# Optimization experiments

Measured on AMD Instinct MI355X. Metric: run time of the kernel, lower is better.

## Reference

```python
import jax, jax.numpy as jnp
import numpy as np

# Dimensions (see shape_source)
N, M, C = 64, 300, 768          # batch, tokens (=max_frames), token dim
LAMB, G, K = 2, 8, 64           # expansion, groups, clusters
GS = LAMB * C // G              # group_size = 192
DESC = K * GS                   # 12288 NeXtVLAD descriptor dim
NB, NCLS = 512, 701             # bottleneck, classes


def setup_inputs() -> dict:
    key = jax.random.key(0)
    ks = jax.random.split(key, 8)
    w = lambda i, shape: jax.random.normal(ks[i], shape, jnp.float32) * 0.02
    return {
        "features": jax.random.normal(ks[0], (N, M + 1, C), jnp.float32),
        # NeXtVLAD_block params
        "fc0_w": w(1, (LAMB * C, C)), "fc0_b": jnp.zeros((LAMB * C,), jnp.float32),
        "fcgk_w": w(2, (G * K, LAMB * C)), "fcgk_b": jnp.zeros((G * K,), jnp.float32),
        "fcg_w": w(3, (G, LAMB * C)), "fcg_b": jnp.zeros((G,), jnp.float32),
        "bn0_g": jnp.ones((M,), jnp.float32), "bn0_b": jnp.zeros((M,), jnp.float32),
        "cw2": jax.random.uniform(ks[4], (1, GS, K), jnp.float32),
        "bn1_g": jnp.ones((1,), jnp.float32), "bn1_b": jnp.zeros((1,), jnp.float32),
        # ClassBlock params (Linear -> BN -> Linear classifier)
        "cls_fc_w": w(5, (NB, DESC)), "cls_fc_b": jnp.zeros((NB,), jnp.float32),
        "cls_bn_g": jnp.ones((NB,), jnp.float32), "cls_bn_b": jnp.zeros((NB,), jnp.float32),
        "cls_w": w(6, (NCLS, NB)), "cls_b": jnp.zeros((NCLS,), jnp.float32),
    }


def reference(features, fc0_w, fc0_b, fcgk_w, fcgk_b, fcg_w, fcg_b,
              bn0_g, bn0_b, cw2, bn1_g, bn1_b,
              cls_fc_w, cls_fc_b, cls_bn_g, cls_bn_b, cls_w, cls_b):
    # Drop CLS token -> local descriptors (N, M, C). (transpose+vector2image
    # in the torch code is a pure rearrangement back to (N, M, C) tokens.)
    x = features[:, 1:]
    # 1) expand D -> lamb*D
    x_dot = jnp.einsum('nmc,ec->nme', x, fc0_w) + fc0_b           # (N, M, lamb*C)
    # 2) group: (N, M*G, group_size)
    x_tilde = x_dot.reshape(-1, M * G, GS)
    # 3) soft assignment logits, BN over the frame axis (inference-mode BN:
    #    running stats 0/1 -> pure per-frame affine), softmax over clusters
    WgkX = jnp.einsum('nme,fe->nmf', x_dot, fcgk_w) + fcgk_b      # (N, M, G*K)
    WgkX = WgkX * bn0_g[None, :, None] + bn0_b[None, :, None]
    alpha_gk = jax.nn.softmax(WgkX.reshape(-1, M * G, K), axis=-1)
    # 4) sigmoid group attention
    alpha_g = jax.nn.sigmoid(jnp.einsum('nme,ge->nmg', x_dot, fcg_w) + fcg_b)
    alpha_g = alpha_g.reshape(-1, M * G, 1)
    activation = alpha_gk * alpha_g                                # (N, M*G, K)
    # 5) aggregate residuals: vlad = act^T x_tilde - a_sum * centers
    a = jnp.sum(activation, axis=1, keepdims=True) * cw2           # (N, GS, K)
    vlad = jnp.einsum('npk,npd->ndk', activation, x_tilde) - a     # (N, GS, K)
    # 6) L1-normalize over group_size dim (F.normalize(vlad, 1): p=1, dim=1)
    norm = jnp.maximum(jnp.sum(jnp.abs(vlad), axis=1, keepdims=True), 1e-12)
    vlad = (vlad / norm).reshape(-1, DESC)
    # bn1 = BatchNorm1d(1), inference mode -> scalar affine
    vlad = vlad * bn1_g[0] + bn1_b[0]
    # ClassBlock: Linear -> BN (inference affine) -> classifier Linear
    f = jnp.einsum('nd,bd->nb', vlad, cls_fc_w) + cls_fc_b         # (N, NB)
    f = f * cls_bn_g + cls_bn_b
    cls = jnp.einsum('nb,cb->nc', f, cls_w) + cls_b                # (N, NCLS)
    return (cls, f)
```

## Files before the change

### kernel.cpp

```cpp
#include <hip/hip_runtime.h>
#include <hip/hip_bf16.h>

#define NN 64
#define MM 300
#define CC 768
#define EE 1536
#define GG 8
#define KK 64
#define FF 512
#define GS 192
#define PP 2400
#define DESC 12288
#define NMROWS 19200
#define NB 512
#define NCLS 701

typedef _Float16 v8h __attribute__((ext_vector_type(8)));
typedef _Float16 v4h __attribute__((ext_vector_type(4)));
typedef float    v4f __attribute__((ext_vector_type(4)));

#define GLOAD_LDS16(g, s) \
    __builtin_amdgcn_global_load_lds( \
        (const __attribute__((address_space(1))) void*)(g), \
        (__attribute__((address_space(3))) void*)(s), 16, 0, 0)

__global__ __launch_bounds__(256)
void pack_x_k(const float* __restrict__ f, _Float16* __restrict__ o)
{
    int idx = blockIdx.x * 256 + threadIdx.x;
    int row = idx / 192;
    int c4  = (idx - row * 192) * 4;
    int n = row / 300, m = row - n * 300;
    float4 v = *(const float4*)(f + ((size_t)(n * 301 + m + 1)) * CC + c4);
    v4h h = { (_Float16)v.x, (_Float16)v.y, (_Float16)v.z, (_Float16)v.w };
    *(v4h*)(o + (size_t)row * CC + c4) = h;
}

__global__ __launch_bounds__(256)
void pack_w_k(const float* __restrict__ s, _Float16* __restrict__ o, int n4)
{
    int idx = blockIdx.x * 256 + threadIdx.x;
    if (idx >= n4) return;
    float4 v = *(const float4*)(s + (size_t)idx * 4);
    v4h h = { (_Float16)v.x, (_Float16)v.y, (_Float16)v.z, (_Float16)v.w };
    *(v4h*)(o + (size_t)idx * 4) = h;
}

__global__ __launch_bounds__(256)
void transpose_w1_k(const float* __restrict__ w1, _Float16* __restrict__ o)
{
    __shared__ float T[64][65];
    const int c0 = blockIdx.x * 64, e0 = blockIdx.y * 64;
    const int tc = threadIdx.x & 63, te = threadIdx.x >> 6;
    #pragma unroll
    for (int r = 0; r < 16; ++r) {
        int el = te * 16 + r;
        T[el][tc] = w1[(size_t)(e0 + el) * CC + c0 + tc];
    }
    __syncthreads();
    #pragma unroll
    for (int r = 0; r < 16; ++r) {
        int cl = te * 16 + r;
        o[(size_t)(c0 + cl) * EE + e0 + tc] = (_Float16)T[tc][cl];
    }
}

__global__ __launch_bounds__(256)
void biasc_k(const float* __restrict__ w2, const float* __restrict__ b2,
             const float* __restrict__ wg, const float* __restrict__ bg,
             const float* __restrict__ b0, float* __restrict__ biasc)
{
    int f = blockIdx.x;
    const float* row = (f < FF) ? (w2 + (size_t)f * EE) : (wg + (size_t)(f - FF) * EE);
    float s = 0.f;
    for (int e = threadIdx.x; e < EE; e += 256) s += row[e] * b0[e];
    __shared__ float red[256];
    red[threadIdx.x] = s;
    __syncthreads();
    for (int o = 128; o; o >>= 1) {
        if (threadIdx.x < o) red[threadIdx.x] += red[threadIdx.x + o];
        __syncthreads();
    }
    if (threadIdx.x == 0)
        biasc[f] = red[0] + ((f < FF) ? b2[f] : bg[f - FF]);
}

__global__ __launch_bounds__(256)
void wgc_k(const float* __restrict__ wg, const float* __restrict__ w1,
           float* __restrict__ wgc)
{
    const int c = blockIdx.x * 64 + (threadIdx.x & 63);
    const int q = threadIdx.x >> 6;
    float acc[GG] = {};
    for (int e = q * 384; e < q * 384 + 384; ++e) {
        float w1v = w1[(size_t)e * CC + c];
        #pragma unroll
        for (int g = 0; g < GG; ++g) acc[g] = fmaf(wg[g * EE + e], w1v, acc[g]);
    }
    __shared__ float red[4][GG][64];
    #pragma unroll
    for (int g = 0; g < GG; ++g) red[q][g][threadIdx.x & 63] = acc[g];
    __syncthreads();
    if (threadIdx.x < 64) {
        #pragma unroll
        for (int g = 0; g < GG; ++g)
            wgc[g * CC + c] = red[0][g][threadIdx.x] + red[1][g][threadIdx.x]
                            + red[2][g][threadIdx.x] + red[3][g][threadIdx.x];
    }
}

template<bool OUTF16, bool BN0, bool SOFTGATE, bool BIAS>
__global__ __launch_bounds__(256)
void hgemm_nt(const _Float16* __restrict__ A, const _Float16* __restrict__ B,
              const float* __restrict__ bias,
              const float* __restrict__ bn_g, const float* __restrict__ bn_b,
              const float* __restrict__ sig,
              void* __restrict__ Cout, int Ndim, int Kdim)
{
    __shared__ _Float16 As[128 * 32];
    __shared__ _Float16 Bs[128 * 32];

    const int tid  = threadIdx.x;
    const int wave = tid >> 6, lane = tid & 63;
    const int wr   = wave >> 1, wc = wave & 1;
    const int row0 = blockIdx.y * 128, col0 = blockIdx.x * 128;

    const int r0 = tid >> 2, cs = tid & 3;
    const int cc = cs ^ ((r0 >> 1) & 3);
    const _Float16* ga0 = A + (size_t)(row0 + r0) * Kdim + cc * 8;
    const _Float16* ga1 = A + (size_t)(row0 + r0 + 64) * Kdim + cc * 8;
    const _Float16* gb0 = B + (size_t)(col0 + r0) * Kdim + cc * 8;
    const _Float16* gb1 = B + (size_t)(col0 + r0 + 64) * Kdim + cc * 8;
    _Float16* sa0 = As + wave * 512;
    _Float16* sa1 = As + 2048 + wave * 512;
    _Float16* sb0 = Bs + wave * 512;
    _Float16* sb1 = Bs + 2048 + wave * 512;

    v4f acc[4][4];
    #pragma unroll
    for (int i = 0; i < 4; ++i)
        #pragma unroll
        for (int j = 0; j < 4; ++j)
            acc[i][j] = (v4f){0.f, 0.f, 0.f, 0.f};

    const int fm = lane & 15, fq = lane >> 4;
    const int sw = (fm >> 1) & 3;
    const _Float16* arp = As + (wr * 64 + fm) * 32 + (fq ^ sw) * 8;
    const _Float16* brp = Bs + (wc * 64 + fm) * 32 + (fq ^ sw) * 8;

    for (int kt = 0; kt < Kdim; kt += 32) {
        GLOAD_LDS16(ga0 + kt, sa0);
        GLOAD_LDS16(ga1 + kt, sa1);
        GLOAD_LDS16(gb0 + kt, sb0);
        GLOAD_LDS16(gb1 + kt, sb1);
        __syncthreads();

        v8h af[4], bf[4];
        #pragma unroll
        for (int i = 0; i < 4; ++i) af[i] = *(const v8h*)(arp + i * 16 * 32);
        #pragma unroll
        for (int j = 0; j < 4; ++j) bf[j] = *(const v8h*)(brp + j * 16 * 32);
        #pragma unroll
        for (int i = 0; i < 4; ++i)
            #pragma unroll
            for (int j = 0; j < 4; ++j)
                acc[i][j] = __builtin_amdgcn_mfma_f32_16x16x32_f16(
                    af[i], bf[j], acc[i][j], 0, 0, 0);
        __syncthreads();
    }

    float bj[4];
    #pragma unroll
    for (int j = 0; j < 4; ++j)
        bj[j] = BIAS ? bias[col0 + wc * 64 + j * 16 + fm] : 0.f;

    if (SOFTGATE) {
        const int gidx = (col0 >> 6) + wc;
        #pragma unroll
        for (int i = 0; i < 4; ++i) {
            #pragma unroll
            for (int r = 0; r < 4; ++r) {
                int grow = row0 + wr * 64 + i * 16 + fq * 4 + r;
                int n = grow / 300, mm = grow - n * 300;
                float g = bn_g[mm], bb = bn_b[mm];
                float v[4];
                #pragma unroll
                for (int j = 0; j < 4; ++j)
                    v[j] = (acc[i][j][r] + bj[j]) * g + bb;
                float mx = fmaxf(fmaxf(v[0], v[1]), fmaxf(v[2], v[3]));
                #pragma unroll
                for (int w = 1; w < 16; w <<= 1) mx = fmaxf(mx, __shfl_xor(mx, w));
                float e[4], s = 0.f;
                #pragma unroll
                for (int j = 0; j < 4; ++j) { e[j] = __expf(v[j] - mx); s += e[j]; }
                #pragma unroll
                for (int w = 1; w < 16; w <<= 1) s += __shfl_xor(s, w);
                float gate = sig[(size_t)grow * GG + gidx];
                float inv = gate / s;
                if (OUTF16) {
                    _Float16* cp = (_Float16*)Cout + (size_t)grow * Ndim + col0 + wc * 64;
                    #pragma unroll
                    for (int j = 0; j < 4; ++j) cp[j * 16 + fm] = (_Float16)(e[j] * inv);
                } else {
                    float* cp = (float*)Cout + (size_t)grow * Ndim + col0 + wc * 64;
                    #pragma unroll
                    for (int j = 0; j < 4; ++j) cp[j * 16 + fm] = e[j] * inv;
                }
            }
        }
        return;
    }

    #pragma unroll
    for (int i = 0; i < 4; ++i) {
        #pragma unroll
        for (int r = 0; r < 4; ++r) {
            int grow = row0 + wr * 64 + i * 16 + fq * 4 + r;
            float g = 1.f, bb = 0.f;
            if (BN0) { int m = grow % 300; g = bn_g[m]; bb = bn_b[m]; }
            #pragma unroll
            for (int j = 0; j < 4; ++j) {
                int gcol = col0 + wc * 64 + j * 16 + fm;
                float v = acc[i][j][r] + bj[j];
                if (BN0) v = v * g + bb;
                if (OUTF16)
                    ((_Float16*)Cout)[(size_t)grow * Ndim + gcol] = (_Float16)v;
                else
                    ((float*)Cout)[(size_t)grow * Ndim + gcol] = v;
            }
        }
    }
}

__global__ __launch_bounds__(256)
void alpha_sig_k(const _Float16* __restrict__ x, const float* __restrict__ wgc,
                 const float* __restrict__ bgc, float* __restrict__ sig)
{
    __shared__ float W[GG * CC];
    for (int i = threadIdx.x; i < GG * CC; i += 256) W[i] = wgc[i];
    __syncthreads();

    const int wave = threadIdx.x >> 6;
    const int lane = threadIdx.x & 63;

    for (int rr = 0; rr < 4; ++rr) {
        int row = blockIdx.x * 16 + wave * 4 + rr;
        const _Float16* xr = x + (size_t)row * CC;
        float acc[GG] = {};
        for (int c = lane; c < CC; c += 64) {
            float xv = (float)xr[c];
            #pragma unroll
            for (int g = 0; g < GG; ++g) acc[g] = fmaf(xv, W[g * CC + c], acc[g]);
        }
        float myval = 0.f;
        #pragma unroll
        for (int g = 0; g < GG; ++g) {
            float s = acc[g];
            #pragma unroll
            for (int o = 32; o; o >>= 1) s += __shfl_xor(s, o);
            if (lane == g) myval = s + bgc[g];
        }
        if (lane < GG) {
            sig[(size_t)row * GG + lane] = 1.f / (1.f + __expf(-myval));
        }
    }
}

__global__ __launch_bounds__(256)
void asum_ps_k(const _Float16* __restrict__ act, float* __restrict__ apart)
{
    const int ps = blockIdx.x, n = blockIdx.y;
    const int k = threadIdx.x & 63, q = threadIdx.x >> 6;
    const _Float16* base = act + ((size_t)n * PP + ps * 300 + q * 75) * 64 + k;
    float s = 0.f;
    for (int p = 0; p < 75; ++p) s += (float)base[(size_t)p * 64];
    __shared__ float part[4][64];
    part[q][k] = s;
    __syncthreads();
    if (threadIdx.x < 64)
        apart[((size_t)ps * NN + n) * 64 + threadIdx.x] =
            part[0][threadIdx.x] + part[1][threadIdx.x]
          + part[2][threadIdx.x] + part[3][threadIdx.x];
}

__global__ __launch_bounds__(256)
void vlad_ps_k(const _Float16* __restrict__ act, const _Float16* __restrict__ xdot,
               float* __restrict__ part)
{
    const int dt = blockIdx.x, n = blockIdx.y, ps = blockIdx.z;
    const int d0 = dt * 64;
    const int p0 = ps * 300, pend = p0 + 300;
    __shared__ float As[16][64];
    __shared__ float Xs[16][64];
    const int tid = threadIdx.x;
    const int tx = tid & 15, ty = tid >> 4;
    const int kb = tx * 4, db = ty * 4;
    const _Float16* actn = act + (size_t)n * PP * 64;
    const _Float16* xn   = xdot + (size_t)n * MM * EE;
    float acc[4][4] = {};

    const int lpp = tid >> 4, lk4 = (tid & 15) << 2;
    for (int pc = p0; pc < pend; pc += 16) {
        int p = pc + lpp;
        float a0 = 0.f, a1 = 0.f, a2 = 0.f, a3 = 0.f;
        float x0 = 0.f, x1 = 0.f, x2 = 0.f, x3 = 0.f;
        if (p < pend) {
            v4h avh = *(const v4h*)(actn + (size_t)p * 64 + lk4);
            a0 = (float)avh[0]; a1 = (float)avh[1]; a2 = (float)avh[2]; a3 = (float)avh[3];
            v4h xv = *(const v4h*)(xn + (size_t)(p >> 3) * EE + (p & 7) * GS + d0 + lk4);
            x0 = (float)xv[0]; x1 = (float)xv[1]; x2 = (float)xv[2]; x3 = (float)xv[3];
        }
        As[lpp][lk4 + 0] = a0; As[lpp][lk4 + 1] = a1;
        As[lpp][lk4 + 2] = a2; As[lpp][lk4 + 3] = a3;
        Xs[lpp][lk4 + 0] = x0; Xs[lpp][lk4 + 1] = x1;
        Xs[lpp][lk4 + 2] = x2; Xs[lpp][lk4 + 3] = x3;
        __syncthreads();
        #pragma unroll
        for (int q = 0; q < 16; ++q) {
            float4 a4 = *(const float4*)&As[q][kb];
            float4 x4 = *(const float4*)&Xs[q][db];
            float aa[4] = {a4.x, a4.y, a4.z, a4.w};
            float xx[4] = {x4.x, x4.y, x4.z, x4.w};
            #pragma unroll
            for (int i = 0; i < 4; ++i)
                #pragma unroll
                for (int j = 0; j < 4; ++j)
                    acc[i][j] = fmaf(xx[i], aa[j], acc[i][j]);
        }
        __syncthreads();
    }

    float* pp = part + ((size_t)ps * NN + n) * DESC;
    #pragma unroll
    for (int i = 0; i < 4; ++i) {
        int dd = d0 + db + i;
        float4 o = {acc[i][0], acc[i][1], acc[i][2], acc[i][3]};
        *(float4*)(pp + (size_t)dd * 64 + kb) = o;
    }
}

__global__ __launch_bounds__(256)
void vlad_reduce_k(const float* __restrict__ part, const float* __restrict__ apart,
                   const float* __restrict__ cw2, float* __restrict__ vlad)
{
    int idx = blockIdx.x * 256 + threadIdx.x;
    float s = 0.f;
    #pragma unroll
    for (int ps = 0; ps < 8; ++ps) s += part[(size_t)ps * (NN * DESC) + idx];
    int k = idx & 63;
    int d = (idx >> 6) % GS;
    int n = idx / DESC;
    float a = 0.f;
    #pragma unroll
    for (int ps = 0; ps < 8; ++ps) a += apart[((size_t)ps * NN + n) * 64 + k];
    vlad[idx] = s - a * cw2[d * 64 + k];
}

__global__ __launch_bounds__(256)
void norm_k(float* __restrict__ vlad, const float* __restrict__ bn1g,
            const float* __restrict__ bn1b)
{
    int n = blockIdx.x;
    float* v = vlad + (size_t)n * DESC;
    int k = threadIdx.x & 63, q = threadIdx.x >> 6;
    float s = 0.f;
    for (int d = q * 48; d < q * 48 + 48; ++d) s += fabsf(v[d * 64 + k]);
    __shared__ float part[4][64];
    __shared__ float inv[64];
    part[q][k] = s;
    __syncthreads();
    if (threadIdx.x < 64) {
        float t = part[0][threadIdx.x] + part[1][threadIdx.x]
                + part[2][threadIdx.x] + part[3][threadIdx.x];
        inv[threadIdx.x] = 1.f / fmaxf(t, 1e-12f);
    }
    __syncthreads();
    float g = bn1g[0], b = bn1b[0];
    for (int idx = threadIdx.x; idx < DESC; idx += 256) {
        v[idx] = v[idx] * inv[idx & 63] * g + b;
    }
}

__global__ __launch_bounds__(256)
void fsplit_k(const float* __restrict__ vlad, const float* __restrict__ W,
              float* __restrict__ part)
{
    const int bcol0 = (blockIdx.x & 7) * 64;
    const int ks = blockIdx.x >> 3;
    const int kc0 = ks * 256;
    __shared__ float Vs[32][68];
    __shared__ float Ws[32][68];
    const int tid = threadIdx.x, tx = tid & 15, ty = tid >> 4;
    float acc[4][4] = {};

    for (int kc = kc0; kc < kc0 + 256; kc += 32) {
        #pragma unroll
        for (int it = 0; it < 2; ++it) {
            int sl = tid + it * 256;
            int rr = sl >> 3, k4 = (sl & 7) << 2;
            float4 v = *(const float4*)(vlad + (size_t)rr * DESC + kc + k4);
            Vs[k4+0][rr] = v.x; Vs[k4+1][rr] = v.y; Vs[k4+2][rr] = v.z; Vs[k4+3][rr] = v.w;
            float4 w = *(const float4*)(W + (size_t)(bcol0 + rr) * DESC + kc + k4);
            Ws[k4+0][rr] = w.x; Ws[k4+1][rr] = w.y; Ws[k4+2][rr] = w.z; Ws[k4+3][rr] = w.w;
        }
        __syncthreads();
        #pragma unroll
        for (int q = 0; q < 32; ++q) {
            float4 wv = *(const float4*)&Ws[q][tx*4];
            float4 vv = *(const float4*)&Vs[q][ty*4];
            float wa[4] = {wv.x, wv.y, wv.z, wv.w};
            float va[4] = {vv.x, vv.y, vv.z, vv.w};
            #pragma unroll
            for (int i = 0; i < 4; ++i)
                #pragma unroll
                for (int j = 0; j < 4; ++j)
                    acc[i][j] = fmaf(va[i], wa[j], acc[i][j]);
        }
        __syncthreads();
    }
    float* p = part + (size_t)ks * (NN * NB);
    #pragma unroll
    for (int i = 0; i < 4; ++i) {
        int n = ty * 4 + i;
        float4 o = {acc[i][0], acc[i][1], acc[i][2], acc[i][3]};
        *(float4*)(p + (size_t)n * NB + bcol0 + tx*4) = o;
    }
}

__global__ __launch_bounds__(256)
void freduce_k(const float* __restrict__ part, const float* __restrict__ bias,
               const float* __restrict__ bng, const float* __restrict__ bnb,
               float* __restrict__ f)
{
    int idx = blockIdx.x * 256 + threadIdx.x;
    float s = 0.f;
    for (int ks = 0; ks < 48; ++ks) s += part[(size_t)ks * (NN * NB) + idx];
    int b = idx & (NB - 1);
    f[idx] = (s + bias[b]) * bng[b] + bnb[b];
}

__global__ __launch_bounds__(256)
void cls_k(const float* __restrict__ f, const float* __restrict__ W,
           const float* __restrict__ bias, float* __restrict__ out)
{
    const int c0 = blockIdx.x * 64;
    __shared__ float Fs[32][68];
    __shared__ float Ws[32][68];
    const int tid = threadIdx.x, tx = tid & 15, ty = tid >> 4;
    float acc[4][4] = {};

    for (int kc = 0; kc < NB; kc += 32) {
        #pragma unroll
        for (int it = 0; it < 2; ++it) {
            int sl = tid + it * 256;
            int rr = sl >> 3, k4 = (sl & 7) << 2;
            float4 v = *(const float4*)(f + (size_t)rr * NB + kc + k4);
            Fs[k4+0][rr] = v.x; Fs[k4+1][rr] = v.y; Fs[k4+2][rr] = v.z; Fs[k4+3][rr] = v.w;
            int c = c0 + rr;
            float4 w = (c < NCLS) ? *(const float4*)(W + (size_t)c * NB + kc + k4)
                                  : make_float4(0.f, 0.f, 0.f, 0.f);
            Ws[k4+0][rr] = w.x; Ws[k4+1][rr] = w.y; Ws[k4+2][rr] = w.z; Ws[k4+3][rr] = w.w;
        }
        __syncthreads();
        #pragma unroll
        for (int q = 0; q < 32; ++q) {
            float4 wv = *(const float4*)&Ws[q][tx*4];
            float4 fv = *(const float4*)&Fs[q][ty*4];
            float wa[4] = {wv.x, wv.y, wv.z, wv.w};
            float fa[4] = {fv.x, fv.y, fv.z, fv.w};
            #pragma unroll
            for (int i = 0; i < 4; ++i)
                #pragma unroll
                for (int j = 0; j < 4; ++j)
                    acc[i][j] = fmaf(fa[i], wa[j], acc[i][j]);
        }
        __syncthreads();
    }
    #pragma unroll
    for (int i = 0; i < 4; ++i) {
        int n = ty * 4 + i;
        #pragma unroll
        for (int j = 0; j < 4; ++j) {
            int c = c0 + tx * 4 + j;
            if (c < NCLS) out[(size_t)n * NCLS + c] = acc[i][j] + bias[c];
        }
    }
}

extern "C" void kernel_launch(void* const* d_in, const int* in_sizes, int n_in,
                              void* d_out, int out_size, void* d_ws, size_t ws_size,
                              hipStream_t stream)
{
    const float* features = (const float*)d_in[0];
    const float* fc0_w    = (const float*)d_in[1];
    const float* fc0_b    = (const float*)d_in[2];
    const float* fcgk_w   = (const float*)d_in[3];
    const float* fcgk_b   = (const float*)d_in[4];
    const float* fcg_w    = (const float*)d_in[5];
    const float* fcg_b    = (const float*)d_in[6];
    const float* bn0_g    = (const float*)d_in[7];
    const float* bn0_b    = (const float*)d_in[8];
    const float* cw2      = (const float*)d_in[9];
    const float* bn1_g    = (const float*)d_in[10];
    const float* bn1_b    = (const float*)d_in[11];
    const float* cls_fc_w = (const float*)d_in[12];
    const float* cls_fc_b = (const float*)d_in[13];
    const float* cls_bn_g = (const float*)d_in[14];
    const float* cls_bn_b = (const float*)d_in[15];
    const float* cls_w    = (const float*)d_in[16];
    const float* cls_b    = (const float*)d_in[17];

    char* ws = (char*)d_ws;
    _Float16* xf16   = (_Float16*)(ws + 0);
    _Float16* w1f16  = (_Float16*)(ws + 29491200);
    _Float16* w2f16  = (_Float16*)(ws + 31850496);
    _Float16* w1t16  = (_Float16*)(ws + 33423360);
    _Float16* w2cf16 = (_Float16*)(ws + 35782656);
    float*    biasc  = (float*)   (ws + 36569088);
    float*    wgc    = (float*)   (ws + 36573184);
    _Float16* xdot16 = (_Float16*)(ws + 36597760);
    _Float16* act16  = (_Float16*)(ws + 95580160);
    float*    sigma  = (float*)   (ws + 115240960);
    float*    apart  = (float*)   (ws + 115855360);
    float*    vpart  = (float*)   (ws + 115986432);
    float*    vlad   = (float*)   (ws + 141152256);
    float*    fpart  = (float*)   (ws + 144297984);

    float* cls_out = (float*)d_out;
    float* f_out   = cls_out + NN * NCLS;

    dim3 blk(256);

    pack_x_k<<<14400, blk, 0, stream>>>(features, xf16);
    pack_w_k<<<1152, blk, 0, stream>>>(fc0_w, w1f16, EE * CC / 4);
    pack_w_k<<<768, blk, 0, stream>>>(fcgk_w, w2f16, FF * EE / 4);
    transpose_w1_k<<<dim3(12, 24), blk, 0, stream>>>(fc0_w, w1t16);
    biasc_k<<<520, blk, 0, stream>>>(fcgk_w, fcgk_b, fcg_w, fcg_b, fc0_b, biasc);
    wgc_k<<<12, blk, 0, stream>>>(fcg_w, fc0_w, wgc);
    hgemm_nt<true, false, false, false><<<dim3(6, 4), blk, 0, stream>>>(
        w2f16, w1t16, nullptr, nullptr, nullptr, nullptr, w2cf16, CC, EE);

    hgemm_nt<true, false, false, true><<<dim3(12, 150), blk, 0, stream>>>(
        xf16, w1f16, fc0_b, nullptr, nullptr, nullptr, xdot16, EE, CC);

    alpha_sig_k<<<1200, blk, 0, stream>>>(xf16, wgc, biasc + FF, sigma);

    hgemm_nt<true, true, true, true><<<dim3(4, 150), blk, 0, stream>>>(
        xf16, w2cf16, biasc, bn0_g, bn0_b, sigma, act16, FF, CC);

    asum_ps_k<<<dim3(8, 64), blk, 0, stream>>>(act16, apart);

    vlad_ps_k<<<dim3(3, 64, 8), blk, 0, stream>>>(act16, xdot16, vpart);
    vlad_reduce_k<<<3072, blk, 0, stream>>>(vpart, apart, cw2, vlad);

    norm_k<<<64, blk, 0, stream>>>(vlad, bn1_g, bn1_b);

    fsplit_k<<<384, blk, 0, stream>>>(vlad, cls_fc_w, fpart);
    freduce_k<<<128, blk, 0, stream>>>(fpart, cls_fc_b, cls_bn_g, cls_bn_b, f_out);

    cls_k<<<11, blk, 0, stream>>>(f_out, cls_w, cls_b, cls_out);
}
```

Measured before the change: 510.7 us.

## Merge setup, alpha, asum and norm kernels; split-K cls and wgc with atomics

Folds the six setup kernels into one block-indexed setup kernel and gives wgc more parallelism through atomic accumulation. The alpha-sigmoid work rides as extra blocks in the xdot GEMM launch, and the activation-sum runs as extra blocks in the VLAD partial kernel. The VLAD reduce and L1 norm become one kernel, and the classifier is split over K with atomics. The aim is fewer launches and better occupancy of small kernels, at the cost of two memsets, float atomics and extra branch-indexed blocks.

Result: faster. 445.9 us (-12.7%).

```diff
diff --git a/kernel.cpp b/kernel.cpp
--- a/kernel.cpp
+++ b/kernel.cpp
@@ -25,105 +25,151 @@
         (__attribute__((address_space(3))) void*)(s), 16, 0, 0)
 
 __global__ __launch_bounds__(256)
-void pack_x_k(const float* __restrict__ f, _Float16* __restrict__ o)
-{
-    int idx = blockIdx.x * 256 + threadIdx.x;
-    int row = idx / 192;
-    int c4  = (idx - row * 192) * 4;
-    int n = row / 300, m = row - n * 300;
-    float4 v = *(const float4*)(f + ((size_t)(n * 301 + m + 1)) * CC + c4);
-    v4h h = { (_Float16)v.x, (_Float16)v.y, (_Float16)v.z, (_Float16)v.w };
-    *(v4h*)(o + (size_t)row * CC + c4) = h;
-}
-
-__global__ __launch_bounds__(256)
-void pack_w_k(const float* __restrict__ s, _Float16* __restrict__ o, int n4)
-{
-    int idx = blockIdx.x * 256 + threadIdx.x;
-    if (idx >= n4) return;
-    float4 v = *(const float4*)(s + (size_t)idx * 4);
-    v4h h = { (_Float16)v.x, (_Float16)v.y, (_Float16)v.z, (_Float16)v.w };
-    *(v4h*)(o + (size_t)idx * 4) = h;
-}
-
-__global__ __launch_bounds__(256)
-void transpose_w1_k(const float* __restrict__ w1, _Float16* __restrict__ o)
-{
-    __shared__ float T[64][65];
-    const int c0 = blockIdx.x * 64, e0 = blockIdx.y * 64;
-    const int tc = threadIdx.x & 63, te = threadIdx.x >> 6;
-    #pragma unroll
-    for (int r = 0; r < 16; ++r) {
-        int el = te * 16 + r;
-        T[el][tc] = w1[(size_t)(e0 + el) * CC + c0 + tc];
-    }
-    __syncthreads();
-    #pragma unroll
-    for (int r = 0; r < 16; ++r) {
-        int cl = te * 16 + r;
-        o[(size_t)(c0 + cl) * EE + e0 + tc] = (_Float16)T[tc][cl];
-    }
-}
-
-__global__ __launch_bounds__(256)
-void biasc_k(const float* __restrict__ w2, const float* __restrict__ b2,
-             const float* __restrict__ wg, const float* __restrict__ bg,
-             const float* __restrict__ b0, float* __restrict__ biasc)
-{
-    int f = blockIdx.x;
-    const float* row = (f < FF) ? (w2 + (size_t)f * EE) : (wg + (size_t)(f - FF) * EE);
-    float s = 0.f;
-    for (int e = threadIdx.x; e < EE; e += 256) s += row[e] * b0[e];
-    __shared__ float red[256];
-    red[threadIdx.x] = s;
-    __syncthreads();
-    for (int o = 128; o; o >>= 1) {
-        if (threadIdx.x < o) red[threadIdx.x] += red[threadIdx.x + o];
-        __syncthreads();
-    }
-    if (threadIdx.x == 0)
-        biasc[f] = red[0] + ((f < FF) ? b2[f] : bg[f - FF]);
-}
-
-__global__ __launch_bounds__(256)
-void wgc_k(const float* __restrict__ wg, const float* __restrict__ w1,
-           float* __restrict__ wgc)
-{
-    const int c = blockIdx.x * 64 + (threadIdx.x & 63);
-    const int q = threadIdx.x >> 6;
-    float acc[GG] = {};
-    for (int e = q * 384; e < q * 384 + 384; ++e) {
-        float w1v = w1[(size_t)e * CC + c];
-        #pragma unroll
-        for (int g = 0; g < GG; ++g) acc[g] = fmaf(wg[g * EE + e], w1v, acc[g]);
-    }
-    __shared__ float red[4][GG][64];
-    #pragma unroll
-    for (int g = 0; g < GG; ++g) red[q][g][threadIdx.x & 63] = acc[g];
-    __syncthreads();
-    if (threadIdx.x < 64) {
-        #pragma unroll
-        for (int g = 0; g < GG; ++g)
-            wgc[g * CC + c] = red[0][g][threadIdx.x] + red[1][g][threadIdx.x]
-                            + red[2][g][threadIdx.x] + red[3][g][threadIdx.x];
-    }
-}
-
-template<bool OUTF16, bool BN0, bool SOFTGATE, bool BIAS>
+void setup_k(const float* __restrict__ features, const float* __restrict__ fc0_w,
+             const float* __restrict__ fcgk_w, const float* __restrict__ fcg_w,
+             const float* __restrict__ fc0_b, const float* __restrict__ fcgk_b,
+             const float* __restrict__ fcg_b,
+             _Float16* __restrict__ xf16, _Float16* __restrict__ w1f16,
+             _Float16* __restrict__ w2f16, _Float16* __restrict__ w1t16,
+             float* __restrict__ biasc, float* __restrict__ wgc)
+{
+    __shared__ __align__(16) char sm[16640];
+    const int bid = blockIdx.x, tid = threadIdx.x;
+
+    if (bid < 14400) {
+        int idx = bid * 256 + tid;
+        int row = idx / 192;
+        int c4  = (idx - row * 192) * 4;
+        int n = row / 300, m = row - n * 300;
+        float4 v = *(const float4*)(features + ((size_t)(n * 301 + m + 1)) * CC + c4);
+        v4h h = { (_Float16)v.x, (_Float16)v.y, (_Float16)v.z, (_Float16)v.w };
+        *(v4h*)(xf16 + (size_t)row * CC + c4) = h;
+        return;
+    }
+    if (bid < 15552) {
+        int idx = (bid - 14400) * 256 + tid;
+        float4 v = *(const float4*)(fc0_w + (size_t)idx * 4);
+        v4h h = { (_Float16)v.x, (_Float16)v.y, (_Float16)v.z, (_Float16)v.w };
+        *(v4h*)(w1f16 + (size_t)idx * 4) = h;
+        return;
+    }
+    if (bid < 16320) {
+        int idx = (bid - 15552) * 256 + tid;
+        float4 v = *(const float4*)(fcgk_w + (size_t)idx * 4);
+        v4h h = { (_Float16)v.x, (_Float16)v.y, (_Float16)v.z, (_Float16)v.w };
+        *(v4h*)(w2f16 + (size_t)idx * 4) = h;
+        return;
+    }
+    if (bid < 16608) {
+        float (*T)[65] = (float(*)[65])sm;
+        int b = bid - 16320;
+        const int c0 = (b % 12) * 64, e0 = (b / 12) * 64;
+        const int tc = tid & 63, te = tid >> 6;
+        #pragma unroll
+        for (int r = 0; r < 16; ++r) {
+            int el = te * 16 + r;
+            T[el][tc] = fc0_w[(size_t)(e0 + el) * CC + c0 + tc];
+        }
+        __syncthreads();
+        #pragma unroll
+        for (int r = 0; r < 16; ++r) {
+            int cl = te * 16 + r;
+            w1t16[(size_t)(c0 + cl) * EE + e0 + tc] = (_Float16)T[tc][cl];
+        }
+        return;
+    }
+    if (bid < 17128) {
+        float* red = (float*)sm;
+        int f = bid - 16608;
+        const float* row = (f < FF) ? (fcgk_w + (size_t)f * EE)
+                                    : (fcg_w + (size_t)(f - FF) * EE);
+        float s = 0.f;
+        for (int e = tid; e < EE; e += 256) s += row[e] * fc0_b[e];
+        red[tid] = s;
+        __syncthreads();
+        for (int o = 128; o; o >>= 1) {
+            if (tid < o) red[tid] += red[tid + o];
+            __syncthreads();
+        }
+        if (tid == 0)
+            biasc[f] = red[0] + ((f < FF) ? fcgk_b[f] : fcg_b[f - FF]);
+        return;
+    }
+    {
+        float (*red)[GG][64] = (float(*)[GG][64])sm;
+        int b = bid - 17128;
+        const int c = (b % 12) * 64 + (tid & 63);
+        const int es = b / 12, q = tid >> 6;
+        float acc[GG] = {};
+        for (int e = es * 192 + q * 48; e < es * 192 + q * 48 + 48; ++e) {
+            float w1v = fc0_w[(size_t)e * CC + c];
+            #pragma unroll
+            for (int g = 0; g < GG; ++g) acc[g] = fmaf(fcg_w[g * EE + e], w1v, acc[g]);
+        }
+        #pragma unroll
+        for (int g = 0; g < GG; ++g) red[q][g][tid & 63] = acc[g];
+        __syncthreads();
+        if (tid < 64) {
+            #pragma unroll
+            for (int g = 0; g < GG; ++g) {
+                float v = red[0][g][tid] + red[1][g][tid] + red[2][g][tid] + red[3][g][tid];
+                atomicAdd(&wgc[g * CC + c], v);
+            }
+        }
+        return;
+    }
+}
+
+template<bool OUTF16, bool BN0, bool SOFTGATE, bool BIAS, bool ALPHA>
 __global__ __launch_bounds__(256)
 void hgemm_nt(const _Float16* __restrict__ A, const _Float16* __restrict__ B,
               const float* __restrict__ bias,
               const float* __restrict__ bn_g, const float* __restrict__ bn_b,
               const float* __restrict__ sig,
-              void* __restrict__ Cout, int Ndim, int Kdim)
-{
-    __shared__ _Float16 As[128 * 32];
-    __shared__ _Float16 Bs[128 * 32];
-
+              void* __restrict__ Cout, int Ndim, int Kdim, int gx,
+              int gemm_blocks,
+              const float* __restrict__ wgc, const float* __restrict__ bgc,
+              float* __restrict__ sigout)
+{
+    __shared__ __align__(16) char smem[24576];
     const int tid  = threadIdx.x;
+    const int bid  = blockIdx.x;
     const int wave = tid >> 6, lane = tid & 63;
-    const int wr   = wave >> 1, wc = wave & 1;
-    const int row0 = blockIdx.y * 128, col0 = blockIdx.x * 128;
+
+    if (ALPHA && bid >= gemm_blocks) {
+        float* Wl = (float*)smem;
+        for (int i = tid; i < GG * CC; i += 256) Wl[i] = wgc[i];
+        __syncthreads();
+        const int abid = bid - gemm_blocks;
+        for (int rr = 0; rr < 4; ++rr) {
+            int row = abid * 16 + wave * 4 + rr;
+            const _Float16* xr = A + (size_t)row * CC;
+            float acc[GG] = {};
+            for (int c = lane; c < CC; c += 64) {
+                float xv = (float)xr[c];
+                #pragma unroll
+                for (int g = 0; g < GG; ++g) acc[g] = fmaf(xv, Wl[g * CC + c], acc[g]);
+            }
+            float myval = 0.f;
+            #pragma unroll
+            for (int g = 0; g < GG; ++g) {
+                float s = acc[g];
+                #pragma unroll
+                for (int o = 32; o; o >>= 1) s += __shfl_xor(s, o);
+                if (lane == g) myval = s + bgc[g];
+            }
+            if (lane < GG)
+                sigout[(size_t)row * GG + lane] = 1.f / (1.f + __expf(-myval));
+        }
+        return;
+    }
+
+    _Float16* As = (_Float16*)smem;
+    _Float16* Bs = (_Float16*)(smem + 8192);
+
+    const int bx = bid % gx, by = bid / gx;
+    const int wr = wave >> 1, wc = wave & 1;
+    const int row0 = by * 128, col0 = bx * 128;
 
     const int r0 = tid >> 2, cs = tid & 3;
     const int cc = cs ^ ((r0 >> 1) & 3);
@@ -197,15 +243,9 @@
                 for (int w = 1; w < 16; w <<= 1) s += __shfl_xor(s, w);
                 float gate = sig[(size_t)grow * GG + gidx];
                 float inv = gate / s;
-                if (OUTF16) {
-                    _Float16* cp = (_Float16*)Cout + (size_t)grow * Ndim + col0 + wc * 64;
-                    #pragma unroll
-                    for (int j = 0; j < 4; ++j) cp[j * 16 + fm] = (_Float16)(e[j] * inv);
-                } else {
-                    float* cp = (float*)Cout + (size_t)grow * Ndim + col0 + wc * 64;
-                    #pragma unroll
-                    for (int j = 0; j < 4; ++j) cp[j * 16 + fm] = e[j] * inv;
-                }
+                _Float16* cp = (_Float16*)Cout + (size_t)grow * Ndim + col0 + wc * 64;
+                #pragma unroll
+                for (int j = 0; j < 4; ++j) cp[j * 16 + fm] = (_Float16)(e[j] * inv);
             }
         }
         return;
@@ -233,66 +273,33 @@
 }
 
 __global__ __launch_bounds__(256)
-void alpha_sig_k(const _Float16* __restrict__ x, const float* __restrict__ wgc,
-                 const float* __restrict__ bgc, float* __restrict__ sig)
-{
-    __shared__ float W[GG * CC];
-    for (int i = threadIdx.x; i < GG * CC; i += 256) W[i] = wgc[i];
-    __syncthreads();
-
-    const int wave = threadIdx.x >> 6;
-    const int lane = threadIdx.x & 63;
-
-    for (int rr = 0; rr < 4; ++rr) {
-        int row = blockIdx.x * 16 + wave * 4 + rr;
-        const _Float16* xr = x + (size_t)row * CC;
-        float acc[GG] = {};
-        for (int c = lane; c < CC; c += 64) {
-            float xv = (float)xr[c];
-            #pragma unroll
-            for (int g = 0; g < GG; ++g) acc[g] = fmaf(xv, W[g * CC + c], acc[g]);
-        }
-        float myval = 0.f;
-        #pragma unroll
-        for (int g = 0; g < GG; ++g) {
-            float s = acc[g];
-            #pragma unroll
-            for (int o = 32; o; o >>= 1) s += __shfl_xor(s, o);
-            if (lane == g) myval = s + bgc[g];
-        }
-        if (lane < GG) {
-            sig[(size_t)row * GG + lane] = 1.f / (1.f + __expf(-myval));
-        }
-    }
-}
-
-__global__ __launch_bounds__(256)
-void asum_ps_k(const _Float16* __restrict__ act, float* __restrict__ apart)
-{
-    const int ps = blockIdx.x, n = blockIdx.y;
-    const int k = threadIdx.x & 63, q = threadIdx.x >> 6;
-    const _Float16* base = act + ((size_t)n * PP + ps * 300 + q * 75) * 64 + k;
-    float s = 0.f;
-    for (int p = 0; p < 75; ++p) s += (float)base[(size_t)p * 64];
-    __shared__ float part[4][64];
-    part[q][k] = s;
-    __syncthreads();
-    if (threadIdx.x < 64)
-        apart[((size_t)ps * NN + n) * 64 + threadIdx.x] =
-            part[0][threadIdx.x] + part[1][threadIdx.x]
-          + part[2][threadIdx.x] + part[3][threadIdx.x];
-}
-
-__global__ __launch_bounds__(256)
-void vlad_ps_k(const _Float16* __restrict__ act, const _Float16* __restrict__ xdot,
-               float* __restrict__ part)
-{
-    const int dt = blockIdx.x, n = blockIdx.y, ps = blockIdx.z;
+void vladact_k(const _Float16* __restrict__ act, const _Float16* __restrict__ xdot,
+               float* __restrict__ part, float* __restrict__ apart)
+{
+    __shared__ __align__(16) char sm[8192];
+    const int tid = threadIdx.x, bid = blockIdx.x;
+
+    if (bid >= 1536) {
+        float (*red)[64] = (float(*)[64])sm;
+        int b = bid - 1536;
+        const int ps = b & 7, n = b >> 3;
+        const int k = tid & 63, q = tid >> 6;
+        const _Float16* base = act + ((size_t)n * PP + ps * 300 + q * 75) * 64 + k;
+        float s = 0.f;
+        for (int p = 0; p < 75; ++p) s += (float)base[(size_t)p * 64];
+        red[q][k] = s;
+        __syncthreads();
+        if (tid < 64)
+            apart[((size_t)ps * NN + n) * 64 + tid] =
+                red[0][tid] + red[1][tid] + red[2][tid] + red[3][tid];
+        return;
+    }
+
+    float (*As)[64] = (float(*)[64])sm;
+    float (*Xs)[64] = (float(*)[64])(sm + 4096);
+    const int dt = bid % 3, n = (bid / 3) & 63, ps = bid / 192;
     const int d0 = dt * 64;
     const int p0 = ps * 300, pend = p0 + 300;
-    __shared__ float As[16][64];
-    __shared__ float Xs[16][64];
-    const int tid = threadIdx.x;
     const int tx = tid & 15, ty = tid >> 4;
     const int kb = tx * 4, db = ty * 4;
     const _Float16* actn = act + (size_t)n * PP * 64;
@@ -340,44 +347,49 @@
 }
 
 __global__ __launch_bounds__(256)
-void vlad_reduce_k(const float* __restrict__ part, const float* __restrict__ apart,
-                   const float* __restrict__ cw2, float* __restrict__ vlad)
-{
-    int idx = blockIdx.x * 256 + threadIdx.x;
-    float s = 0.f;
-    #pragma unroll
-    for (int ps = 0; ps < 8; ++ps) s += part[(size_t)ps * (NN * DESC) + idx];
-    int k = idx & 63;
-    int d = (idx >> 6) % GS;
-    int n = idx / DESC;
+void vladnorm_k(const float* __restrict__ part, const float* __restrict__ apart,
+                const float* __restrict__ cw2, const float* __restrict__ bn1g,
+                const float* __restrict__ bn1b, float* __restrict__ vlad)
+{
+    const int n = blockIdx.x >> 2, kq = blockIdx.x & 3;
+    const int tk = threadIdx.x & 15, td = threadIdx.x >> 4;
+    const int k = kq * 16 + tk;
+
     float a = 0.f;
     #pragma unroll
     for (int ps = 0; ps < 8; ++ps) a += apart[((size_t)ps * NN + n) * 64 + k];
-    vlad[idx] = s - a * cw2[d * 64 + k];
-}
-
-__global__ __launch_bounds__(256)
-void norm_k(float* __restrict__ vlad, const float* __restrict__ bn1g,
-            const float* __restrict__ bn1b)
-{
-    int n = blockIdx.x;
-    float* v = vlad + (size_t)n * DESC;
-    int k = threadIdx.x & 63, q = threadIdx.x >> 6;
-    float s = 0.f;
-    for (int d = q * 48; d < q * 48 + 48; ++d) s += fabsf(v[d * 64 + k]);
-    __shared__ float part[4][64];
-    __shared__ float inv[64];
-    part[q][k] = s;
+
+    float vloc[12];
+    float sabs = 0.f;
+    #pragma unroll
+    for (int i = 0; i < 12; ++i) {
+        int d = td * 12 + i;
+        float s = 0.f;
+        #pragma unroll
+        for (int ps = 0; ps < 8; ++ps)
+            s += part[((size_t)ps * NN + n) * DESC + (size_t)d * 64 + k];
+        float v = s - a * cw2[d * 64 + k];
+        vloc[i] = v;
+        sabs += fabsf(v);
+    }
+
+    __shared__ float red[16][16];
+    __shared__ float inv[16];
+    red[td][tk] = sabs;
     __syncthreads();
-    if (threadIdx.x < 64) {
-        float t = part[0][threadIdx.x] + part[1][threadIdx.x]
-                + part[2][threadIdx.x] + part[3][threadIdx.x];
-        inv[threadIdx.x] = 1.f / fmaxf(t, 1e-12f);
+    if (td == 0) {
+        float t = 0.f;
+        #pragma unroll
+        for (int q = 0; q < 16; ++q) t += red[q][tk];
+        inv[tk] = 1.f / fmaxf(t, 1e-12f);
     }
     __syncthreads();
-    float g = bn1g[0], b = bn1b[0];
-    for (int idx = threadIdx.x; idx < DESC; idx += 256) {
-        v[idx] = v[idx] * inv[idx & 63] * g + b;
+    const float g = bn1g[0], b = bn1b[0];
+    const float sc = inv[tk] * g;
+    #pragma unroll
+    for (int i = 0; i < 12; ++i) {
+        int d = td * 12 + i;
+        vlad[(size_t)n * DESC + (size_t)d * 64 + k] = vloc[i] * sc + b;
     }
 }
 
@@ -443,13 +455,14 @@
 void cls_k(const float* __restrict__ f, const float* __restrict__ W,
            const float* __restrict__ bias, float* __restrict__ out)
 {
-    const int c0 = blockIdx.x * 64;
+    const int c0 = (blockIdx.x % 11) * 64;
+    const int ks = blockIdx.x / 11;
     __shared__ float Fs[32][68];
     __shared__ float Ws[32][68];
     const int tid = threadIdx.x, tx = tid & 15, ty = tid >> 4;
     float acc[4][4] = {};
 
-    for (int kc = 0; kc < NB; kc += 32) {
+    for (int kc = ks * 128; kc < ks * 128 + 128; kc += 32) {
         #pragma unroll
         for (int it = 0; it < 2; ++it) {
             int sl = tid + it * 256;
@@ -482,7 +495,10 @@
         #pragma unroll
         for (int j = 0; j < 4; ++j) {
             int c = c0 + tx * 4 + j;
-            if (c < NCLS) out[(size_t)n * NCLS + c] = acc[i][j] + bias[c];
+            if (c < NCLS) {
+                float v = acc[i][j] + ((ks == 0) ? bias[c] : 0.f);
+                atomicAdd(&out[(size_t)n * NCLS + c], v);
+            }
         }
     }
 }
@@ -531,32 +547,31 @@
 
     dim3 blk(256);
 
-    pack_x_k<<<14400, blk, 0, stream>>>(features, xf16);
-    pack_w_k<<<1152, blk, 0, stream>>>(fc0_w, w1f16, EE * CC / 4);
-    pack_w_k<<<768, blk, 0, stream>>>(fcgk_w, w2f16, FF * EE / 4);
-    transpose_w1_k<<<dim3(12, 24), blk, 0, stream>>>(fc0_w, w1t16);
-    biasc_k<<<520, blk, 0, stream>>>(fcgk_w, fcgk_b, fcg_w, fcg_b, fc0_b, biasc);
-    wgc_k<<<12, blk, 0, stream>>>(fcg_w, fc0_w, wgc);
-    hgemm_nt<true, false, false, false><<<dim3(6, 4), blk, 0, stream>>>(
-        w2f16, w1t16, nullptr, nullptr, nullptr, nullptr, w2cf16, CC, EE);
-
-    hgemm_nt<true, false, false, true><<<dim3(12, 150), blk, 0, stream>>>(
-        xf16, w1f16, fc0_b, nullptr, nullptr, nullptr, xdot16, EE, CC);
-
-    alpha_sig_k<<<1200, blk, 0, stream>>>(xf16, wgc, biasc + FF, sigma);
-
-    hgemm_nt<true, true, true, true><<<dim3(4, 150), blk, 0, stream>>>(
-        xf16, w2cf16, biasc, bn0_g, bn0_b, sigma, act16, FF, CC);
-
-    asum_ps_k<<<dim3(8, 64), blk, 0, stream>>>(act16, apart);
-
-    vlad_ps_k<<<dim3(3, 64, 8), blk, 0, stream>>>(act16, xdot16, vpart);
-    vlad_reduce_k<<<3072, blk, 0, stream>>>(vpart, apart, cw2, vlad);
-
-    norm_k<<<64, blk, 0, stream>>>(vlad, bn1_g, bn1_b);
+    hipMemsetAsync(wgc, 0, GG * CC * sizeof(float), stream);
+    hipMemsetAsync(cls_out, 0, (size_t)NN * NCLS * sizeof(float), stream);
+
+    setup_k<<<17224, blk, 0, stream>>>(features, fc0_w, fcgk_w, fcg_w,
+                                       fc0_b, fcgk_b, fcg_b,
+                                       xf16, w1f16, w2f16, w1t16, biasc, wgc);
+
+    hgemm_nt<true, false, false, false, false><<<24, blk, 0, stream>>>(
+        w2f16, w1t16, nullptr, nullptr, nullptr, nullptr, w2cf16,
+        CC, EE, 6, 0, nullptr, nullptr, nullptr);
+
+    hgemm_nt<true, false, false, true, true><<<1800 + 1200, blk, 0, stream>>>(
+        xf16, w1f16, fc0_b, nullptr, nullptr, nullptr, xdot16,
+        EE, CC, 12, 1800, wgc, biasc + FF, sigma);
+
+    hgemm_nt<true, true, true, true, false><<<600, blk, 0, stream>>>(
+        xf16, w2cf16, biasc, bn0_g, bn0_b, sigma, act16,
+        FF, CC, 4, 0, nullptr, nullptr, nullptr);
+
+    vladact_k<<<2048, blk, 0, stream>>>(act16, xdot16, vpart, apart);
+
+    vladnorm_k<<<256, blk, 0, stream>>>(vpart, apart, cw2, bn1_g, bn1_b, vlad);
 
     fsplit_k<<<384, blk, 0, stream>>>(vlad, cls_fc_w, fpart);
     freduce_k<<<128, blk, 0, stream>>>(fpart, cls_fc_b, cls_bn_g, cls_bn_b, f_out);
 
-    cls_k<<<11, blk, 0, stream>>>(f_out, cls_w, cls_b, cls_out);
-}
+    cls_k<<<44, blk, 0, stream>>>(f_out, cls_w, cls_b, cls_out);
+}
```
